# Performance work log

Measured on AMD Instinct MI355X. Metric: run time of the kernel, lower is better.

## Reference

```python
import jax, jax.numpy as jnp
import numpy as np

B, S, D, H = 2, 2048, 1024, 16
DH = D // H  # head_dim = 64


def setup_inputs() -> dict:
    key = jax.random.key(0)
    ks = jax.random.split(key, 12)
    sd = 0.02
    return {
        "query": jax.random.normal(ks[0], (B, S, D), jnp.float32),
        "value": jax.random.normal(ks[1], (B, S, D), jnp.float32),
        "Wq": jax.random.normal(ks[2], (D, D), jnp.float32) * sd,
        "bq": jnp.zeros((D,), jnp.float32),
        "Wk": jax.random.normal(ks[3], (D, DH), jnp.float32) * sd,
        "bk": jnp.zeros((DH,), jnp.float32),
        "Wv": jax.random.normal(ks[4], (D, DH), jnp.float32) * sd,
        "bv": jnp.zeros((DH,), jnp.float32),
        "Wo": jax.random.normal(ks[5], (D, D), jnp.float32) * sd,
        "bo": jnp.zeros((D,), jnp.float32),
    }


def reference(query, value, Wq, bq, Wk, bk, Wv, bv, Wo, bo):
    b, s, d = query.shape
    # per-head queries: (B, H, S, DH)
    Q = (query @ Wq + bq).reshape(b, s, H, DH).transpose(0, 2, 1, 3)
    # single shared K/V head: (B, S, DH)
    K = value @ Wk + bk
    V = value @ Wv + bv
    scale = 1.0 / jnp.sqrt(jnp.asarray(DH, Q.dtype))
    # broadcast shared K over all query heads: (B, H, S, S)
    scores = jnp.einsum("bhsd,btd->bhst", Q, K) * scale
    weights = jax.nn.softmax(scores, axis=-1)
    # (B, H, S, DH)
    attn = jnp.einsum("bhst,btd->bhsd", weights, V)
    concat = attn.transpose(0, 2, 1, 3).reshape(b, s, d)
    return concat @ Wo + bo
```

## Files before the change

### kernel.cpp

```cpp
#include <hip/hip_runtime.h>
#include <hip/hip_bf16.h>
#include <cstdint>

#define S_LEN 2048
#define D_MODEL 1024
#define NHEAD 16
#define DHEAD 64
#define BATCH 2

typedef __attribute__((ext_vector_type(4))) __bf16 bf16x4v;
typedef __attribute__((ext_vector_type(8))) __bf16 bf16x8v;
typedef __attribute__((ext_vector_type(16))) float f32x16;
typedef const __attribute__((address_space(1))) uint32_t gu32;
typedef __attribute__((address_space(3))) uint32_t lu32;

#define QSCALE 0.18033688011112042f

__device__ __forceinline__ int perm4(int gidx) {
    return (gidx & ~3) | ((gidx & 1) << 1) | ((gidx >> 1) & 1);
}
__device__ __forceinline__ int permk(int k) {
    return (k & ~12) | ((k & 4) << 1) | ((k & 8) >> 1);
}

__global__ __launch_bounds__(256) void prep_cvt(
    const float* __restrict__ qin, const float* __restrict__ vin,
    __hip_bfloat16* __restrict__ Qo, __hip_bfloat16* __restrict__ Vo, int n4each)
{
    const int i = blockIdx.x * 256 + threadIdx.x;
    const float* src;
    __hip_bfloat16* dst;
    int idx;
    if (i < n4each) { src = qin; dst = Qo; idx = i; }
    else            { src = vin; dst = Vo; idx = i - n4each; if (idx >= n4each) return; }
    const float4 v = reinterpret_cast<const float4*>(src)[idx];
    bf16x4v o = { (__bf16)v.x, (__bf16)v.y, (__bf16)v.z, (__bf16)v.w };
    *reinterpret_cast<bf16x4v*>(dst + (size_t)perm4(idx) * 4) = o;
}

__global__ __launch_bounds__(256) void wtrans_all(
    const float* __restrict__ Wq, const float* __restrict__ Wo,
    const float* __restrict__ Wk, const float* __restrict__ Wv,
    __hip_bfloat16* __restrict__ Wqt, __hip_bfloat16* __restrict__ Wohit,
    __hip_bfloat16* __restrict__ Wkvt)
{
    const int z = blockIdx.z;
    const float* W;
    __hip_bfloat16* T;
    int wcols, trowoff;
    if (z == 0)      { W = Wq; T = Wqt;   wcols = 1024; trowoff = 0; }
    else if (z == 1) { W = Wo; T = Wohit; wcols = 1024; trowoff = 0; }
    else if (z == 2) { W = Wk; T = Wkvt;  wcols = 64;   trowoff = 0; }
    else             { W = Wv; T = Wkvt;  wcols = 64;   trowoff = 64; }
    const int bx = blockIdx.x, by = blockIdx.y;
    if (bx * 32 >= wcols) return;

    __shared__ float ld[32][33];
    const int tid = threadIdx.x;
    const int jj = tid & 31;
#pragma unroll
    for (int ii = 0; ii < 4; ++ii) {
        const int rr = (tid >> 5) * 4 + ii;
        ld[rr][jj] = W[(size_t)(by * 32 + rr) * wcols + bx * 32 + jj];
    }
    __syncthreads();
#pragma unroll
    for (int ii = 0; ii < 4; ++ii) {
        const int rr = (tid >> 5) * 4 + ii;
        T[(size_t)(trowoff + bx * 32 + rr) * 1024 + by * 32 + permk(jj)] =
            __float2bfloat16(ld[jj][rr]);
    }
}

template<bool FUSED, bool PERMC, typename OutT>
__global__ __launch_bounds__(512, 1) void gemm_mfma(
    const __hip_bfloat16* __restrict__ Ahi, const __hip_bfloat16* __restrict__ Alo,
    const __hip_bfloat16* __restrict__ Bhi,
    const float* __restrict__ bias, OutT* __restrict__ C, float oscale)
{
    constexpr int NT = 16;
    constexpr int NBUF = FUSED ? 3 : 4;
    constexpr int BUFSZ = FUSED ? 49152 : 32768;
    __shared__ __align__(16) char lds[NBUF * BUFSZ];

    const int tid = threadIdx.x;
    const int w = tid >> 6, lane = tid & 63;
    const int g = lane >> 5, r = lane & 31;
    const int wr = w >> 2, wc = w & 3;
    const int lin = blockIdx.y * 8 + blockIdx.x;
    const int swz = (lin & 7) * 32 + (lin >> 3);
    const int rowBase = (swz >> 3) * 128;
    const int colBase = (swz & 7) * 128;

    auto stage = [&](int buf, int t) {
        const int kk = t * 64;
        char* dst = lds + buf * BUFSZ;
#pragma unroll
        for (int j = 0; j < 2; ++j) {
            const int oo  = j * 8192 + tid * 16;
            const int row = oo >> 7;
            const int cb  = (oo & 127) ^ ((row & 7) << 4);
            __builtin_amdgcn_global_load_lds(
                (gu32*)((const char*)Ahi + (size_t)(rowBase + row) * 2048 + kk * 2 + cb),
                (lu32*)(dst + oo), 16, 0, 0);
            if (FUSED)
                __builtin_amdgcn_global_load_lds(
                    (gu32*)((const char*)Alo + (size_t)(rowBase + row) * 2048 + kk * 2 + cb),
                    (lu32*)(dst + 16384 + oo), 16, 0, 0);
            __builtin_amdgcn_global_load_lds(
                (gu32*)((const char*)Bhi + (size_t)(colBase + row) * 2048 + kk * 2 + cb),
                (lu32*)(dst + (FUSED ? 32768 : 16384) + oo), 16, 0, 0);
        }
    };

    f32x16 acc[2];
#pragma unroll
    for (int i = 0; i < 16; ++i) { acc[0][i] = 0.f; acc[1][i] = 0.f; }

    if (FUSED) { stage(0, 0); stage(1, 1); }
    else       { stage(0, 0); stage(1, 1); stage(2, 2); }

    int b_cur = 0, b_nxt = 1, b_stg = 2;

    for (int t = 0; t < NT; ++t) {
        if (FUSED) {
            if (t < 15) { asm volatile("s_waitcnt vmcnt(6)" ::: "memory"); }
            else        { asm volatile("s_waitcnt vmcnt(0)" ::: "memory"); }
        } else {
            if (t <= 13)      { asm volatile("s_waitcnt vmcnt(8)" ::: "memory"); }
            else if (t == 14) { asm volatile("s_waitcnt vmcnt(4)" ::: "memory"); }
            else              { asm volatile("s_waitcnt vmcnt(0)" ::: "memory"); }
        }
        asm volatile("s_barrier" ::: "memory");

        if (FUSED) { if (t + 2 < NT) stage(b_stg, t + 2); }
        else       { if (t + 3 < NT) stage((t + 3) & 3, t + 3); }

        const int cbuf = FUSED ? b_cur : (t & 3);
        const char* ahb = lds + cbuf * BUFSZ;
        const char* alb = ahb + 16384;
        const char* bb  = ahb + (FUSED ? 32768 : 16384);

        __builtin_amdgcn_s_setprio(1);
#pragma unroll
        for (int ks = 0; ks < 4; ++ks) {
            bf16x8v a[2], bfr;
#pragma unroll
            for (int mt = 0; mt < 2; ++mt) {
                const int rowl = wr * 64 + mt * 32 + r;
                const int sz = (rowl & 7) << 4;
                a[mt] = *reinterpret_cast<const bf16x8v*>(
                    ahb + rowl * 128 + ((ks * 32 + g * 16) ^ sz));
            }
            {
                const int rowl = wc * 32 + r;
                const int sz = (rowl & 7) << 4;
                bfr = *reinterpret_cast<const bf16x8v*>(
                    bb + rowl * 128 + ((ks * 32 + g * 16) ^ sz));
            }
#pragma unroll
            for (int mt = 0; mt < 2; ++mt)
                acc[mt] = __builtin_amdgcn_mfma_f32_32x32x16_bf16(a[mt], bfr, acc[mt], 0, 0, 0);
            if (FUSED) {
                bf16x8v a2[2];
#pragma unroll
                for (int mt = 0; mt < 2; ++mt) {
                    const int rowl = wr * 64 + mt * 32 + r;
                    const int sz = (rowl & 7) << 4;
                    a2[mt] = *reinterpret_cast<const bf16x8v*>(
                        alb + rowl * 128 + ((ks * 32 + g * 16) ^ sz));
                }
#pragma unroll
                for (int mt = 0; mt < 2; ++mt)
                    acc[mt] = __builtin_amdgcn_mfma_f32_32x32x16_bf16(a2[mt], bfr, acc[mt], 0, 0, 0);
            }
        }
        __builtin_amdgcn_s_setprio(0);

        if (FUSED) { const int tmp = b_cur; b_cur = b_nxt; b_nxt = b_stg; b_stg = tmp; }
    }

    const int col = colBase + wc * 32 + r;
    const int colp = PERMC ? permk(col) : col;
    const float bv = bias[col];
#pragma unroll
    for (int mt = 0; mt < 2; ++mt)
#pragma unroll
        for (int reg = 0; reg < 16; ++reg) {
            const int row = rowBase + wr * 64 + mt * 32 + (reg & 3) + 8 * (reg >> 2) + 4 * g;
            C[(size_t)row * 1024 + colp] = static_cast<OutT>((acc[mt][reg] + bv) * oscale);
        }
}

__global__ __launch_bounds__(256) void proj_kv_mfma(
    const __hip_bfloat16* __restrict__ Vbf,
    const __hip_bfloat16* __restrict__ Wkvt,
    const float* __restrict__ bk, const float* __restrict__ bv,
    __hip_bfloat16* __restrict__ Kb,
    __hip_bfloat16* __restrict__ Vt)
{
    __shared__ __align__(16) char lds[40960];
    const int tid = threadIdx.x;
    const int w = tid >> 6, lane = tid & 63;
    const int g = lane >> 5, r = lane & 31;
    const int rowBase = blockIdx.x * 32;

    auto stage = [&](int buf, int t) {
        const int kk = t * 64;
        char* dst = lds + buf * 20480;
        {
            const int oo  = tid * 16;
            const int row = oo >> 7;
            const int cb  = (oo & 127) ^ ((row & 7) << 4);
            __builtin_amdgcn_global_load_lds(
                (gu32*)((const char*)Vbf + (size_t)(rowBase + row) * 2048 + kk * 2 + cb),
                (lu32*)(dst + oo), 16, 0, 0);
        }
#pragma unroll
        for (int j = 0; j < 4; ++j) {
            const int oo  = j * 4096 + tid * 16;
            const int row = oo >> 7;
            const int cb  = (oo & 127) ^ ((row & 7) << 4);
            __builtin_amdgcn_global_load_lds(
                (gu32*)((const char*)Wkvt + (size_t)row * 2048 + kk * 2 + cb),
                (lu32*)(dst + 4096 + oo), 16, 0, 0);
        }
    };

    f32x16 acc;
#pragma unroll
    for (int i = 0; i < 16; ++i) acc[i] = 0.f;

    stage(0, 0);

    for (int t = 0; t < 16; ++t) {
        const int cur = t & 1;
        if (t < 15) {
            stage(cur ^ 1, t + 1);
            asm volatile("s_waitcnt vmcnt(5)" ::: "memory");
        } else {
            asm volatile("s_waitcnt vmcnt(0)" ::: "memory");
        }
        asm volatile("s_barrier" ::: "memory");

        const char* ab = lds + cur * 20480;
        const char* bb = ab + 4096;

#pragma unroll
        for (int ks = 0; ks < 4; ++ks) {
            const int sza = (r & 7) << 4;
            bf16x8v af = *reinterpret_cast<const bf16x8v*>(
                ab + r * 128 + ((ks * 32 + g * 16) ^ sza));
            bf16x8v bf = *reinterpret_cast<const bf16x8v*>(
                bb + (w * 32 + r) * 128 + ((ks * 32 + g * 16) ^ sza));
            acc = __builtin_amdgcn_mfma_f32_32x32x16_bf16(af, bf, acc, 0, 0, 0);
        }
        asm volatile("s_barrier" ::: "memory");
    }

    __syncthreads();
    float* ep = reinterpret_cast<float*>(lds);
#pragma unroll
    for (int reg = 0; reg < 16; ++reg) {
        const int m = (reg & 3) + 8 * (reg >> 2) + 4 * g;
        ep[m * 132 + w * 32 + r] = acc[reg];
    }
    __syncthreads();

    {
        const int m  = tid >> 3;
        const int g0 = (tid & 7) * 2;
#pragma unroll
        for (int j = 0; j < 2; ++j) {
            const int gsrc = g0 + j;
            bf16x4v o4;
#pragma unroll
            for (int i2 = 0; i2 < 4; ++i2)
                o4[i2] = (__bf16)(ep[m * 132 + gsrc * 4 + i2] + bk[gsrc * 4 + i2]);
            *reinterpret_cast<bf16x4v*>(
                Kb + (size_t)(rowBase + m) * 64 + perm4(gsrc) * 4) = o4;
        }
    }
    {
        const int vc = tid >> 2;
        const int g0 = (tid & 3) * 2;
        const int batch = rowBase >> 11;
        const float bvv = bv[vc];
#pragma unroll
        for (int j = 0; j < 2; ++j) {
            const int gsrc = g0 + j;
            bf16x4v o4;
#pragma unroll
            for (int i2 = 0; i2 < 4; ++i2)
                o4[i2] = (__bf16)(ep[(gsrc * 4 + i2) * 132 + 64 + vc] + bvv);
            *reinterpret_cast<bf16x4v*>(
                Vt + ((size_t)(batch * 64 + vc)) * 2048 + (rowBase & 2047) + perm4(gsrc) * 4) = o4;
        }
    }
}

__global__ __launch_bounds__(256, 2) void mqa_attn_mfma(
    const __hip_bfloat16* __restrict__ Qbf,
    const __hip_bfloat16* __restrict__ Kbf,
    const __hip_bfloat16* __restrict__ Vt,
    __hip_bfloat16* __restrict__ Ahi,
    __hip_bfloat16* __restrict__ Alo)
{
    __shared__ __align__(16) char lds[65536];

    const int bh = blockIdx.y, b = bh >> 4, h = bh & 15;
    const int qt = blockIdx.x;
    const int tid = threadIdx.x;
    const int w = tid >> 6, lane = tid & 63;
    const int g = lane >> 5, q = lane & 31;

    bf16x8v qf[4];
    {
        const __hip_bfloat16* qp =
            Qbf + ((size_t)(b * S_LEN + qt * 128 + w * 32 + q)) * D_MODEL + h * DHEAD;
#pragma unroll
        for (int ks = 0; ks < 4; ++ks)
            qf[ks] = *reinterpret_cast<const bf16x8v*>(qp + ks * 16 + g * 8);
    }

    const bf16x8v onesf = {(__bf16)1.f, (__bf16)1.f, (__bf16)1.f, (__bf16)1.f,
                           (__bf16)1.f, (__bf16)1.f, (__bf16)1.f, (__bf16)1.f};
    f32x16 fzero;
#pragma unroll
    for (int i = 0; i < 16; ++i) fzero[i] = 0.f;

    const char* kbase = (const char*)Kbf + (size_t)b * S_LEN * DHEAD * 2;
    const char* vbase = (const char*)Vt + (size_t)b * DHEAD * S_LEN * 2;

    auto stage = [&](int buf, int t0) {
        char* dst = lds + buf * 16384;
#pragma unroll
        for (int j = 0; j < 2; ++j) {
            const int oo = j * 4096 + tid * 16;
            const int rr = oo >> 7;
            const int cc = (oo & 127) ^ ((rr & 7) << 4);
            __builtin_amdgcn_global_load_lds(
                (gu32*)(kbase + (size_t)(t0 + rr) * 128 + cc),
                (lu32*)(dst + oo), 16, 0, 0);
            __builtin_amdgcn_global_load_lds(
                (gu32*)(vbase + (size_t)rr * (S_LEN * 2) + t0 * 2 + cc),
                (lu32*)(dst + 8192 + oo), 16, 0, 0);
        }
    };

    f32x16 oacc[2], oacc_l;
#pragma unroll
    for (int i = 0; i < 16; ++i) { oacc[0][i] = 0.f; oacc[1][i] = 0.f; oacc_l[i] = 0.f; }

    auto qkt = [&](f32x16 (&SD)[2], int buf) {
        const char* kb_ = lds + buf * 16384;
#pragma unroll
        for (int mt = 0; mt < 2; ++mt) {
            const int key = mt * 32 + q;
            const char* krow = kb_ + key * 128;
            const int swz = (key & 7) << 4;
            bf16x8v af0 = *reinterpret_cast<const bf16x8v*>(krow + ((g * 16) ^ swz));
            SD[mt] = __builtin_amdgcn_mfma_f32_32x32x16_bf16(af0, qf[0], fzero, 0, 0, 0);
#pragma unroll
            for (int ks = 1; ks < 4; ++ks) {
                bf16x8v af = *reinterpret_cast<const bf16x8v*>(
                    krow + ((ks * 32 + g * 16) ^ swz));
                SD[mt] = __builtin_amdgcn_mfma_f32_32x32x16_bf16(af, qf[ks], SD[mt], 0, 0, 0);
            }
        }
    };

    auto smpv = [&](f32x16 (&SD)[2], int buf) {
#pragma unroll
        for (int mt = 0; mt < 2; ++mt)
#pragma unroll
            for (int r2 = 0; r2 < 16; ++r2)
                SD[mt][r2] = exp2f(SD[mt][r2]);

        bf16x8v pf[4];
#pragma unroll
        for (int ks = 0; ks < 4; ++ks)
#pragma unroll
            for (int e2 = 0; e2 < 8; ++e2)
                pf[ks][e2] = (__bf16)SD[ks >> 1][(ks & 1) * 8 + e2];

        const char* vb_ = lds + buf * 16384 + 8192;
#pragma unroll
        for (int mt = 0; mt < 2; ++mt) {
            const int drow = mt * 32 + q;
            const char* vrow = vb_ + drow * 128;
            const int swz = (drow & 7) << 4;
#pragma unroll
            for (int ks = 0; ks < 4; ++ks) {
                bf16x8v af = *reinterpret_cast<const bf16x8v*>(
                    vrow + ((ks * 32 + g * 16) ^ swz));
                oacc[mt] = __builtin_amdgcn_mfma_f32_32x32x16_bf16(af, pf[ks], oacc[mt], 0, 0, 0);
            }
        }
#pragma unroll
        for (int ks = 0; ks < 4; ++ks)
            oacc_l = __builtin_amdgcn_mfma_f32_32x32x16_bf16(onesf, pf[ks], oacc_l, 0, 0, 0);
    };

    f32x16 sA[2], sB[2];

    stage(0, 0); stage(1, 64); stage(2, 128);
    asm volatile("s_waitcnt vmcnt(8)" ::: "memory");
    asm volatile("s_barrier" ::: "memory");
    qkt(sA, 0);

#define BODY(SB_, TILE_, BQ_, BP_, CUR, NXT, VMCSTR, DOSTAGE)               \
    {                                                                        \
        asm volatile("s_waitcnt vmcnt(" VMCSTR ")" ::: "memory");            \
        asm volatile("s_barrier" ::: "memory");                              \
        if (DOSTAGE) stage(SB_, TILE_);                                      \
        qkt(NXT, BQ_);                                                       \
        smpv(CUR, BP_);                                                      \
    }

    for (int ib = 0; ib < 7; ++ib) {
        const int t4 = ib * 4;
        BODY(3, (t4 + 3) * 64, 1, 0, sA, sB, "4", true);
        BODY(0, (t4 + 4) * 64, 2, 1, sB, sA, "4", true);
        BODY(1, (t4 + 5) * 64, 3, 2, sA, sB, "4", true);
        BODY(2, (t4 + 6) * 64, 0, 3, sB, sA, "4", true);
    }
    BODY(3, 31 * 64, 1, 0, sA, sB, "4", true);
    BODY(0, 0,       2, 1, sB, sA, "4", false);
    BODY(0, 0,       3, 2, sA, sB, "0", false);
#undef BODY
    smpv(sB, 3);

    const float inv = 1.f / oacc_l[0];
    __syncthreads();
    {
        float* ep = reinterpret_cast<float*>(lds) + w * 2080;
#pragma unroll
        for (int mt = 0; mt < 2; ++mt)
#pragma unroll
            for (int r = 0; r < 16; ++r) {
                const int d = mt * 32 + (r & 3) + ((r >> 2) * 8) + g * 4;
                ep[q * 65 + d] = oacc[mt][r] * inv;
            }
    }
    __syncthreads();

    const size_t obase = (size_t)(b * S_LEN + qt * 128) * D_MODEL + h * DHEAD;
    for (int i = tid; i < 128 * 16; i += 256) {
        const int rloc = i >> 4, G = i & 15;
        const float* src = reinterpret_cast<float*>(lds) + (rloc >> 5) * 2080 + (rloc & 31) * 65 + G * 4;
        const size_t o = obase + (size_t)rloc * D_MODEL + perm4(G) * 4;
        bf16x4v hv, lv;
#pragma unroll
        for (int j = 0; j < 4; ++j) {
            const float v = src[j];
            const float h2 = __bfloat162float(__float2bfloat16(v));
            hv[j] = (__bf16)h2;
            lv[j] = (__bf16)(v - h2);
        }
        *reinterpret_cast<bf16x4v*>(Ahi + o) = hv;
        *reinterpret_cast<bf16x4v*>(Alo + o) = lv;
    }
}

extern "C" void kernel_launch(void* const* d_in, const int* in_sizes, int n_in,
                              void* d_out, int out_size, void* d_ws, size_t ws_size,
                              hipStream_t stream)
{
    const float* query = (const float*)d_in[0];
    const float* value = (const float*)d_in[1];
    const float* Wq    = (const float*)d_in[2];
    const float* bq    = (const float*)d_in[3];
    const float* Wk    = (const float*)d_in[4];
    const float* bk    = (const float*)d_in[5];
    const float* Wv    = (const float*)d_in[6];
    const float* bv    = (const float*)d_in[7];
    const float* Wo    = (const float*)d_in[8];
    const float* bo    = (const float*)d_in[9];
    float* out = (float*)d_out;

    const int BS = BATCH * S_LEN;
    char* ws = (char*)d_ws;
    const size_t MB = 1024 * 1024;
    __hip_bfloat16* Qin   = (__hip_bfloat16*)(ws);
    __hip_bfloat16* AhiB  = (__hip_bfloat16*)(ws);
    __hip_bfloat16* Wqt   = (__hip_bfloat16*)(ws + 8 * MB);
    __hip_bfloat16* Vbf   = (__hip_bfloat16*)(ws + 10 * MB);
    __hip_bfloat16* Qbf   = (__hip_bfloat16*)(ws + 10 * MB);
    __hip_bfloat16* AloB  = (__hip_bfloat16*)(ws + 10 * MB);
    __hip_bfloat16* Kbf   = (__hip_bfloat16*)(ws + 18 * MB);
    __hip_bfloat16* Vt    = (__hip_bfloat16*)(ws + 18 * MB + 524288);
    __hip_bfloat16* Wohit = (__hip_bfloat16*)(ws + 19 * MB);
    __hip_bfloat16* Wkvt  = (__hip_bfloat16*)(ws + 21 * MB);

    const int n4each = BS * D_MODEL / 4;
    prep_cvt<<<dim3(2 * n4each / 256), dim3(256), 0, stream>>>(
        query, value, Qin, Vbf, n4each);
    wtrans_all<<<dim3(32, 32, 4), dim3(256), 0, stream>>>(
        Wq, Wo, Wk, Wv, Wqt, Wohit, Wkvt);

    proj_kv_mfma<<<dim3(BS / 32), dim3(256), 0, stream>>>(Vbf, Wkvt, bk, bv, Kbf, Vt);

    gemm_mfma<false, true, __hip_bfloat16><<<dim3(8, 32), dim3(512), 0, stream>>>(
        Qin, Qin, Wqt, bq, Qbf, QSCALE);

    mqa_attn_mfma<<<dim3(S_LEN / 128, BATCH * NHEAD), dim3(256), 0, stream>>>(
        Qbf, Kbf, Vt, AhiB, AloB);

    gemm_mfma<true, false, float><<<dim3(8, 32), dim3(512), 0, stream>>>(
        AhiB, AloB, Wohit, bo, out, 1.0f);
}
```

Measured before the change: 114.5 us.

## Fuse prep kernels and run KV projection alongside Q projection in one launch

Merges the query conversion and weight transposes into a single launch, and drops the separate bf16 conversion of the value input: the KV projection now reads fp32 value directly and converts to bf16 in registers. The KV projection blocks are packed into the same grid as the Q projection GEMM, so both run concurrently in one launch instead of two serial ones. The attention kernel also precomputes its swizzled K/V LDS offsets. This removes two launches and a full fp32-to-bf16 pass over value, at the cost of heterogeneous blocks sharing one large LDS allocation and extra fp32 traffic in the KV blocks.

```diff
diff --git a/kernel.cpp b/kernel.cpp
--- a/kernel.cpp
+++ b/kernel.cpp
@@ -23,28 +23,25 @@
     return (k & ~12) | ((k & 4) << 1) | ((k & 8) >> 1);
 }
 
-__global__ __launch_bounds__(256) void prep_cvt(
-    const float* __restrict__ qin, const float* __restrict__ vin,
-    __hip_bfloat16* __restrict__ Qo, __hip_bfloat16* __restrict__ Vo, int n4each)
-{
-    const int i = blockIdx.x * 256 + threadIdx.x;
-    const float* src;
-    __hip_bfloat16* dst;
-    int idx;
-    if (i < n4each) { src = qin; dst = Qo; idx = i; }
-    else            { src = vin; dst = Vo; idx = i - n4each; if (idx >= n4each) return; }
-    const float4 v = reinterpret_cast<const float4*>(src)[idx];
-    bf16x4v o = { (__bf16)v.x, (__bf16)v.y, (__bf16)v.z, (__bf16)v.w };
-    *reinterpret_cast<bf16x4v*>(dst + (size_t)perm4(idx) * 4) = o;
-}
-
-__global__ __launch_bounds__(256) void wtrans_all(
+__global__ __launch_bounds__(256) void prep_all(
+    const float* __restrict__ query,
     const float* __restrict__ Wq, const float* __restrict__ Wo,
     const float* __restrict__ Wk, const float* __restrict__ Wv,
+    __hip_bfloat16* __restrict__ Qin,
     __hip_bfloat16* __restrict__ Wqt, __hip_bfloat16* __restrict__ Wohit,
     __hip_bfloat16* __restrict__ Wkvt)
 {
-    const int z = blockIdx.z;
+    const int bid = blockIdx.x;
+    const int tid = threadIdx.x;
+    if (bid < 4096) {
+        const int idx = bid * 256 + tid;
+        const float4 v = reinterpret_cast<const float4*>(query)[idx];
+        bf16x4v o = { (__bf16)v.x, (__bf16)v.y, (__bf16)v.z, (__bf16)v.w };
+        *reinterpret_cast<bf16x4v*>(Qin + (size_t)perm4(idx) * 4) = o;
+        return;
+    }
+    const int b2 = bid - 4096;
+    const int bx = b2 & 31, by = (b2 >> 5) & 31, z = b2 >> 10;
     const float* W;
     __hip_bfloat16* T;
     int wcols, trowoff;
@@ -52,11 +49,9 @@
     else if (z == 1) { W = Wo; T = Wohit; wcols = 1024; trowoff = 0; }
     else if (z == 2) { W = Wk; T = Wkvt;  wcols = 64;   trowoff = 0; }
     else             { W = Wv; T = Wkvt;  wcols = 64;   trowoff = 64; }
-    const int bx = blockIdx.x, by = blockIdx.y;
     if (bx * 32 >= wcols) return;
 
     __shared__ float ld[32][33];
-    const int tid = threadIdx.x;
     const int jj = tid & 31;
 #pragma unroll
     for (int ii = 0; ii < 4; ++ii) {
@@ -72,16 +67,216 @@
     }
 }
 
-template<bool FUSED, bool PERMC, typename OutT>
-__global__ __launch_bounds__(512, 1) void gemm_mfma(
+__global__ __launch_bounds__(512, 1) void qproj_projkv(
+    const __hip_bfloat16* __restrict__ Qin,
+    const __hip_bfloat16* __restrict__ Wqt,
+    const float* __restrict__ bq,
+    __hip_bfloat16* __restrict__ Qbf,
+    const float* __restrict__ value,
+    const __hip_bfloat16* __restrict__ Wkvt,
+    const float* __restrict__ bk, const float* __restrict__ bv,
+    __hip_bfloat16* __restrict__ Kb,
+    __hip_bfloat16* __restrict__ Vt)
+{
+    __shared__ __align__(16) char lds[131072];
+    const int bid = blockIdx.x;
+    const int tid = threadIdx.x;
+
+    if (bid < 64) {
+        const int unit = tid >> 8;
+        const int ltid = tid & 255;
+        const int w = ltid >> 6, lane = ltid & 63;
+        const int g = lane >> 5, r = lane & 31;
+        const int rowBase = bid * 64 + unit * 32;
+        char* ub = lds + unit * 65536;
+
+        auto stage = [&](int buf, int t) {
+            const int kk = t * 64;
+            char* dst = ub + buf * 24576;
+#pragma unroll
+            for (int j = 0; j < 2; ++j) {
+                const int oo  = j * 4096 + ltid * 16;
+                const int row = oo >> 8;
+                const int cb  = (oo & 255) ^ ((row & 7) << 4);
+                __builtin_amdgcn_global_load_lds(
+                    (gu32*)((const char*)value + (size_t)(rowBase + row) * 4096 + kk * 4 + cb),
+                    (lu32*)(dst + oo), 16, 0, 0);
+            }
+#pragma unroll
+            for (int j = 0; j < 4; ++j) {
+                const int oo  = j * 4096 + ltid * 16;
+                const int row = oo >> 7;
+                const int cb  = (oo & 127) ^ ((row & 7) << 4);
+                __builtin_amdgcn_global_load_lds(
+                    (gu32*)((const char*)Wkvt + (size_t)row * 2048 + kk * 2 + cb),
+                    (lu32*)(dst + 8192 + oo), 16, 0, 0);
+            }
+        };
+
+        f32x16 acc;
+#pragma unroll
+        for (int i = 0; i < 16; ++i) acc[i] = 0.f;
+
+        stage(0, 0);
+
+        for (int t = 0; t < 16; ++t) {
+            const int cur = t & 1;
+            if (t < 15) {
+                stage(cur ^ 1, t + 1);
+                asm volatile("s_waitcnt vmcnt(6)" ::: "memory");
+            } else {
+                asm volatile("s_waitcnt vmcnt(0)" ::: "memory");
+            }
+            asm volatile("s_barrier" ::: "memory");
+
+            const char* ab = ub + cur * 24576;
+            const char* bb = ab + 8192;
+
+#pragma unroll
+            for (int ks = 0; ks < 4; ++ks) {
+                const int sza = (r & 7) << 4;
+                const char* pa = ab + r * 256;
+                const float4 x0 = *reinterpret_cast<const float4*>(
+                    pa + ((ks * 64 + g * 16) ^ sza));
+                const float4 x1 = *reinterpret_cast<const float4*>(
+                    pa + ((ks * 64 + 32 + g * 16) ^ sza));
+                bf16x8v af = {(__bf16)x0.x, (__bf16)x0.y, (__bf16)x0.z, (__bf16)x0.w,
+                              (__bf16)x1.x, (__bf16)x1.y, (__bf16)x1.z, (__bf16)x1.w};
+                bf16x8v bf = *reinterpret_cast<const bf16x8v*>(
+                    bb + (w * 32 + r) * 128 + ((ks * 32 + g * 16) ^ sza));
+                acc = __builtin_amdgcn_mfma_f32_32x32x16_bf16(af, bf, acc, 0, 0, 0);
+            }
+            asm volatile("s_barrier" ::: "memory");
+        }
+
+        __syncthreads();
+        float* ep = reinterpret_cast<float*>(ub);
+#pragma unroll
+        for (int reg = 0; reg < 16; ++reg) {
+            const int m = (reg & 3) + 8 * (reg >> 2) + 4 * g;
+            ep[m * 132 + w * 32 + r] = acc[reg];
+        }
+        __syncthreads();
+
+        {
+            const int m  = ltid >> 3;
+            const int g0 = (ltid & 7) * 2;
+#pragma unroll
+            for (int j = 0; j < 2; ++j) {
+                const int gsrc = g0 + j;
+                bf16x4v o4;
+#pragma unroll
+                for (int i2 = 0; i2 < 4; ++i2)
+                    o4[i2] = (__bf16)(ep[m * 132 + gsrc * 4 + i2] + bk[gsrc * 4 + i2]);
+                *reinterpret_cast<bf16x4v*>(
+                    Kb + (size_t)(rowBase + m) * 64 + perm4(gsrc) * 4) = o4;
+            }
+        }
+        {
+            const int vc = ltid >> 2;
+            const int g0 = (ltid & 3) * 2;
+            const int batch = rowBase >> 11;
+            const float bvv = bv[vc];
+#pragma unroll
+            for (int j = 0; j < 2; ++j) {
+                const int gsrc = g0 + j;
+                bf16x4v o4;
+#pragma unroll
+                for (int i2 = 0; i2 < 4; ++i2)
+                    o4[i2] = (__bf16)(ep[(gsrc * 4 + i2) * 132 + 64 + vc] + bvv);
+                *reinterpret_cast<bf16x4v*>(
+                    Vt + ((size_t)(batch * 64 + vc)) * 2048 + (rowBase & 2047) + perm4(gsrc) * 4) = o4;
+            }
+        }
+        return;
+    }
+
+    const int lin = bid - 64;
+    const int w = tid >> 6, lane = tid & 63;
+    const int g = lane >> 5, r = lane & 31;
+    const int wr = w >> 2, wc = w & 3;
+    const int swz = (lin & 7) * 32 + (lin >> 3);
+    const int rowBase = (swz >> 3) * 128;
+    const int colBase = (swz & 7) * 128;
+
+    auto stage = [&](int buf, int t) {
+        const int kk = t * 64;
+        char* dst = lds + buf * 32768;
+#pragma unroll
+        for (int j = 0; j < 2; ++j) {
+            const int oo  = j * 8192 + tid * 16;
+            const int row = oo >> 7;
+            const int cb  = (oo & 127) ^ ((row & 7) << 4);
+            __builtin_amdgcn_global_load_lds(
+                (gu32*)((const char*)Qin + (size_t)(rowBase + row) * 2048 + kk * 2 + cb),
+                (lu32*)(dst + oo), 16, 0, 0);
+            __builtin_amdgcn_global_load_lds(
+                (gu32*)((const char*)Wqt + (size_t)(colBase + row) * 2048 + kk * 2 + cb),
+                (lu32*)(dst + 16384 + oo), 16, 0, 0);
+        }
+    };
+
+    f32x16 acc[2];
+#pragma unroll
+    for (int i = 0; i < 16; ++i) { acc[0][i] = 0.f; acc[1][i] = 0.f; }
+
+    stage(0, 0); stage(1, 1); stage(2, 2);
+
+    for (int t = 0; t < 16; ++t) {
+        if (t <= 13)      { asm volatile("s_waitcnt vmcnt(8)" ::: "memory"); }
+        else if (t == 14) { asm volatile("s_waitcnt vmcnt(4)" ::: "memory"); }
+        else              { asm volatile("s_waitcnt vmcnt(0)" ::: "memory"); }
+        asm volatile("s_barrier" ::: "memory");
+
+        if (t + 3 < 16) stage((t + 3) & 3, t + 3);
+
+        const char* ahb = lds + (t & 3) * 32768;
+        const char* bb  = ahb + 16384;
+
+        __builtin_amdgcn_s_setprio(1);
+#pragma unroll
+        for (int ks = 0; ks < 4; ++ks) {
+            bf16x8v a[2], bfr;
+#pragma unroll
+            for (int mt = 0; mt < 2; ++mt) {
+                const int rowl = wr * 64 + mt * 32 + r;
+                const int sz = (rowl & 7) << 4;
+                a[mt] = *reinterpret_cast<const bf16x8v*>(
+                    ahb + rowl * 128 + ((ks * 32 + g * 16) ^ sz));
+            }
+            {
+                const int rowl = wc * 32 + r;
+                const int sz = (rowl & 7) << 4;
+                bfr = *reinterpret_cast<const bf16x8v*>(
+                    bb + rowl * 128 + ((ks * 32 + g * 16) ^ sz));
+            }
+#pragma unroll
+            for (int mt = 0; mt < 2; ++mt)
+                acc[mt] = __builtin_amdgcn_mfma_f32_32x32x16_bf16(a[mt], bfr, acc[mt], 0, 0, 0);
+        }
+        __builtin_amdgcn_s_setprio(0);
+    }
+
+    const int col = colBase + wc * 32 + r;
+    const int colp = permk(col);
+    const float bvv = bq[col];
+#pragma unroll
+    for (int mt = 0; mt < 2; ++mt)
+#pragma unroll
+        for (int reg = 0; reg < 16; ++reg) {
+            const int row = rowBase + wr * 64 + mt * 32 + (reg & 3) + 8 * (reg >> 2) + 4 * g;
+            Qbf[(size_t)row * 1024 + colp] =
+                (__hip_bfloat16)((acc[mt][reg] + bvv) * QSCALE);
+        }
+}
+
+__global__ __launch_bounds__(512, 1) void gemm_oproj(
     const __hip_bfloat16* __restrict__ Ahi, const __hip_bfloat16* __restrict__ Alo,
     const __hip_bfloat16* __restrict__ Bhi,
-    const float* __restrict__ bias, OutT* __restrict__ C, float oscale)
+    const float* __restrict__ bias, float* __restrict__ C)
 {
-    constexpr int NT = 16;
-    constexpr int NBUF = FUSED ? 3 : 4;
-    constexpr int BUFSZ = FUSED ? 49152 : 32768;
-    __shared__ __align__(16) char lds[NBUF * BUFSZ];
+    constexpr int BUFSZ = 49152;
+    __shared__ __align__(16) char lds[147456];
 
     const int tid = threadIdx.x;
     const int w = tid >> 6, lane = tid & 63;
@@ -103,13 +298,12 @@
             __builtin_amdgcn_global_load_lds(
                 (gu32*)((const char*)Ahi + (size_t)(rowBase + row) * 2048 + kk * 2 + cb),
                 (lu32*)(dst + oo), 16, 0, 0);
-            if (FUSED)
-                __builtin_amdgcn_global_load_lds(
-                    (gu32*)((const char*)Alo + (size_t)(rowBase + row) * 2048 + kk * 2 + cb),
-                    (lu32*)(dst + 16384 + oo), 16, 0, 0);
+            __builtin_amdgcn_global_load_lds(
+                (gu32*)((const char*)Alo + (size_t)(rowBase + row) * 2048 + kk * 2 + cb),
+                (lu32*)(dst + 16384 + oo), 16, 0, 0);
             __builtin_amdgcn_global_load_lds(
                 (gu32*)((const char*)Bhi + (size_t)(colBase + row) * 2048 + kk * 2 + cb),
-                (lu32*)(dst + (FUSED ? 32768 : 16384) + oo), 16, 0, 0);
+                (lu32*)(dst + 32768 + oo), 16, 0, 0);
         }
     };
 
@@ -117,40 +311,32 @@
 #pragma unroll
     for (int i = 0; i < 16; ++i) { acc[0][i] = 0.f; acc[1][i] = 0.f; }
 
-    if (FUSED) { stage(0, 0); stage(1, 1); }
-    else       { stage(0, 0); stage(1, 1); stage(2, 2); }
-
+    stage(0, 0); stage(1, 1);
     int b_cur = 0, b_nxt = 1, b_stg = 2;
 
-    for (int t = 0; t < NT; ++t) {
-        if (FUSED) {
-            if (t < 15) { asm volatile("s_waitcnt vmcnt(6)" ::: "memory"); }
-            else        { asm volatile("s_waitcnt vmcnt(0)" ::: "memory"); }
-        } else {
-            if (t <= 13)      { asm volatile("s_waitcnt vmcnt(8)" ::: "memory"); }
-            else if (t == 14) { asm volatile("s_waitcnt vmcnt(4)" ::: "memory"); }
-            else              { asm volatile("s_waitcnt vmcnt(0)" ::: "memory"); }
-        }
+    for (int t = 0; t < 16; ++t) {
+        if (t < 15) { asm volatile("s_waitcnt vmcnt(6)" ::: "memory"); }
+        else        { asm volatile("s_waitcnt vmcnt(0)" ::: "memory"); }
         asm volatile("s_barrier" ::: "memory");
 
-        if (FUSED) { if (t + 2 < NT) stage(b_stg, t + 2); }
-        else       { if (t + 3 < NT) stage((t + 3) & 3, t + 3); }
-
-        const int cbuf = FUSED ? b_cur : (t & 3);
-        const char* ahb = lds + cbuf * BUFSZ;
+        if (t + 2 < 16) stage(b_stg, t + 2);
+
+        const char* ahb = lds + b_cur * BUFSZ;
         const char* alb = ahb + 16384;
-        const char* bb  = ahb + (FUSED ? 32768 : 16384);
+        const char* bb  = ahb + 32768;
 
         __builtin_amdgcn_s_setprio(1);
 #pragma unroll
         for (int ks = 0; ks < 4; ++ks) {
-            bf16x8v a[2], bfr;
+            bf16x8v a[2], a2[2], bfr;
 #pragma unroll
             for (int mt = 0; mt < 2; ++mt) {
                 const int rowl = wr * 64 + mt * 32 + r;
                 const int sz = (rowl & 7) << 4;
-                a[mt] = *reinterpret_cast<const bf16x8v*>(
+                a[mt]  = *reinterpret_cast<const bf16x8v*>(
                     ahb + rowl * 128 + ((ks * 32 + g * 16) ^ sz));
+                a2[mt] = *reinterpret_cast<const bf16x8v*>(
+                    alb + rowl * 128 + ((ks * 32 + g * 16) ^ sz));
             }
             {
                 const int rowl = wc * 32 + r;
@@ -159,144 +345,25 @@
                     bb + rowl * 128 + ((ks * 32 + g * 16) ^ sz));
             }
 #pragma unroll
-            for (int mt = 0; mt < 2; ++mt)
-                acc[mt] = __builtin_amdgcn_mfma_f32_32x32x16_bf16(a[mt], bfr, acc[mt], 0, 0, 0);
-            if (FUSED) {
-                bf16x8v a2[2];
-#pragma unroll
-                for (int mt = 0; mt < 2; ++mt) {
-                    const int rowl = wr * 64 + mt * 32 + r;
-                    const int sz = (rowl & 7) << 4;
-                    a2[mt] = *reinterpret_cast<const bf16x8v*>(
-                        alb + rowl * 128 + ((ks * 32 + g * 16) ^ sz));
-                }
-#pragma unroll
-                for (int mt = 0; mt < 2; ++mt)
-                    acc[mt] = __builtin_amdgcn_mfma_f32_32x32x16_bf16(a2[mt], bfr, acc[mt], 0, 0, 0);
+            for (int mt = 0; mt < 2; ++mt) {
+                acc[mt] = __builtin_amdgcn_mfma_f32_32x32x16_bf16(a[mt],  bfr, acc[mt], 0, 0, 0);
+                acc[mt] = __builtin_amdgcn_mfma_f32_32x32x16_bf16(a2[mt], bfr, acc[mt], 0, 0, 0);
             }
         }
         __builtin_amdgcn_s_setprio(0);
 
-        if (FUSED) { const int tmp = b_cur; b_cur = b_nxt; b_nxt = b_stg; b_stg = tmp; }
+        const int tmp = b_cur; b_cur = b_nxt; b_nxt = b_stg; b_stg = tmp;
     }
 
     const int col = colBase + wc * 32 + r;
-    const int colp = PERMC ? permk(col) : col;
-    const float bv = bias[col];
+    const float bvv = bias[col];
 #pragma unroll
     for (int mt = 0; mt < 2; ++mt)
 #pragma unroll
         for (int reg = 0; reg < 16; ++reg) {
             const int row = rowBase + wr * 64 + mt * 32 + (reg & 3) + 8 * (reg >> 2) + 4 * g;
-            C[(size_t)row * 1024 + colp] = static_cast<OutT>((acc[mt][reg] + bv) * oscale);
-        }
-}
-
-__global__ __launch_bounds__(256) void proj_kv_mfma(
-    const __hip_bfloat16* __restrict__ Vbf,
-    const __hip_bfloat16* __restrict__ Wkvt,
-    const float* __restrict__ bk, const float* __restrict__ bv,
-    __hip_bfloat16* __restrict__ Kb,
-    __hip_bfloat16* __restrict__ Vt)
-{
-    __shared__ __align__(16) char lds[40960];
-    const int tid = threadIdx.x;
-    const int w = tid >> 6, lane = tid & 63;
-    const int g = lane >> 5, r = lane & 31;
-    const int rowBase = blockIdx.x * 32;
-
-    auto stage = [&](int buf, int t) {
-        const int kk = t * 64;
-        char* dst = lds + buf * 20480;
-        {
-            const int oo  = tid * 16;
-            const int row = oo >> 7;
-            const int cb  = (oo & 127) ^ ((row & 7) << 4);
-            __builtin_amdgcn_global_load_lds(
-                (gu32*)((const char*)Vbf + (size_t)(rowBase + row) * 2048 + kk * 2 + cb),
-                (lu32*)(dst + oo), 16, 0, 0);
-        }
-#pragma unroll
-        for (int j = 0; j < 4; ++j) {
-            const int oo  = j * 4096 + tid * 16;
-            const int row = oo >> 7;
-            const int cb  = (oo & 127) ^ ((row & 7) << 4);
-            __builtin_amdgcn_global_load_lds(
-                (gu32*)((const char*)Wkvt + (size_t)row * 2048 + kk * 2 + cb),
-                (lu32*)(dst + 4096 + oo), 16, 0, 0);
-        }
-    };
-
-    f32x16 acc;
-#pragma unroll
-    for (int i = 0; i < 16; ++i) acc[i] = 0.f;
-
-    stage(0, 0);
-
-    for (int t = 0; t < 16; ++t) {
-        const int cur = t & 1;
-        if (t < 15) {
-            stage(cur ^ 1, t + 1);
-            asm volatile("s_waitcnt vmcnt(5)" ::: "memory");
-        } else {
-            asm volatile("s_waitcnt vmcnt(0)" ::: "memory");
-        }
-        asm volatile("s_barrier" ::: "memory");
-
-        const char* ab = lds + cur * 20480;
-        const char* bb = ab + 4096;
-
-#pragma unroll
-        for (int ks = 0; ks < 4; ++ks) {
-            const int sza = (r & 7) << 4;
-            bf16x8v af = *reinterpret_cast<const bf16x8v*>(
-                ab + r * 128 + ((ks * 32 + g * 16) ^ sza));
-            bf16x8v bf = *reinterpret_cast<const bf16x8v*>(
-                bb + (w * 32 + r) * 128 + ((ks * 32 + g * 16) ^ sza));
-            acc = __builtin_amdgcn_mfma_f32_32x32x16_bf16(af, bf, acc, 0, 0, 0);
-        }
-        asm volatile("s_barrier" ::: "memory");
-    }
-
-    __syncthreads();
-    float* ep = reinterpret_cast<float*>(lds);
-#pragma unroll
-    for (int reg = 0; reg < 16; ++reg) {
-        const int m = (reg & 3) + 8 * (reg >> 2) + 4 * g;
-        ep[m * 132 + w * 32 + r] = acc[reg];
-    }
-    __syncthreads();
-
-    {
-        const int m  = tid >> 3;
-        const int g0 = (tid & 7) * 2;
-#pragma unroll
-        for (int j = 0; j < 2; ++j) {
-            const int gsrc = g0 + j;
-            bf16x4v o4;
-#pragma unroll
-            for (int i2 = 0; i2 < 4; ++i2)
-                o4[i2] = (__bf16)(ep[m * 132 + gsrc * 4 + i2] + bk[gsrc * 4 + i2]);
-            *reinterpret_cast<bf16x4v*>(
-                Kb + (size_t)(rowBase + m) * 64 + perm4(gsrc) * 4) = o4;
-        }
-    }
-    {
-        const int vc = tid >> 2;
-        const int g0 = (tid & 3) * 2;
-        const int batch = rowBase >> 11;
-        const float bvv = bv[vc];
-#pragma unroll
-        for (int j = 0; j < 2; ++j) {
-            const int gsrc = g0 + j;
-            bf16x4v o4;
-#pragma unroll
-            for (int i2 = 0; i2 < 4; ++i2)
-                o4[i2] = (__bf16)(ep[(gsrc * 4 + i2) * 132 + 64 + vc] + bvv);
-            *reinterpret_cast<bf16x4v*>(
-                Vt + ((size_t)(batch * 64 + vc)) * 2048 + (rowBase & 2047) + perm4(gsrc) * 4) = o4;
-        }
-    }
+            C[(size_t)row * 1024 + col] = acc[mt][reg] + bvv;
+        }
 }
 
 __global__ __launch_bounds__(256, 2) void mqa_attn_mfma(
@@ -329,6 +396,18 @@
 #pragma unroll
     for (int i = 0; i < 16; ++i) fzero[i] = 0.f;
 
+    int koff[2][4], voff[2][4];
+#pragma unroll
+    for (int mt = 0; mt < 2; ++mt) {
+        const int key = mt * 32 + q;
+        const int swzk = (key & 7) << 4;
+#pragma unroll
+        for (int ks = 0; ks < 4; ++ks) {
+            koff[mt][ks] = key * 128 + ((ks * 32 + g * 16) ^ swzk);
+            voff[mt][ks] = 8192 + key * 128 + ((ks * 32 + g * 16) ^ swzk);
+        }
+    }
+
     const char* kbase = (const char*)Kbf + (size_t)b * S_LEN * DHEAD * 2;
     const char* vbase = (const char*)Vt + (size_t)b * DHEAD * S_LEN * 2;
 
@@ -356,15 +435,11 @@
         const char* kb_ = lds + buf * 16384;
 #pragma unroll
         for (int mt = 0; mt < 2; ++mt) {
-            const int key = mt * 32 + q;
-            const char* krow = kb_ + key * 128;
-            const int swz = (key & 7) << 4;
-            bf16x8v af0 = *reinterpret_cast<const bf16x8v*>(krow + ((g * 16) ^ swz));
+            bf16x8v af0 = *reinterpret_cast<const bf16x8v*>(kb_ + koff[mt][0]);
             SD[mt] = __builtin_amdgcn_mfma_f32_32x32x16_bf16(af0, qf[0], fzero, 0, 0, 0);
 #pragma unroll
             for (int ks = 1; ks < 4; ++ks) {
-                bf16x8v af = *reinterpret_cast<const bf16x8v*>(
-                    krow + ((ks * 32 + g * 16) ^ swz));
+                bf16x8v af = *reinterpret_cast<const bf16x8v*>(kb_ + koff[mt][ks]);
                 SD[mt] = __builtin_amdgcn_mfma_f32_32x32x16_bf16(af, qf[ks], SD[mt], 0, 0, 0);
             }
         }
@@ -384,16 +459,12 @@
             for (int e2 = 0; e2 < 8; ++e2)
                 pf[ks][e2] = (__bf16)SD[ks >> 1][(ks & 1) * 8 + e2];
 
-        const char* vb_ = lds + buf * 16384 + 8192;
+        const char* kb_ = lds + buf * 16384;
 #pragma unroll
         for (int mt = 0; mt < 2; ++mt) {
-            const int drow = mt * 32 + q;
-            const char* vrow = vb_ + drow * 128;
-            const int swz = (drow & 7) << 4;
 #pragma unroll
             for (int ks = 0; ks < 4; ++ks) {
-                bf16x8v af = *reinterpret_cast<const bf16x8v*>(
-                    vrow + ((ks * 32 + g * 16) ^ swz));
+                bf16x8v af = *reinterpret_cast<const bf16x8v*>(kb_ + voff[mt][ks]);
                 oacc[mt] = __builtin_amdgcn_mfma_f32_32x32x16_bf16(af, pf[ks], oacc[mt], 0, 0, 0);
             }
         }
@@ -479,13 +550,11 @@
     const float* bo    = (const float*)d_in[9];
     float* out = (float*)d_out;
 
-    const int BS = BATCH * S_LEN;
     char* ws = (char*)d_ws;
     const size_t MB = 1024 * 1024;
     __hip_bfloat16* Qin   = (__hip_bfloat16*)(ws);
     __hip_bfloat16* AhiB  = (__hip_bfloat16*)(ws);
     __hip_bfloat16* Wqt   = (__hip_bfloat16*)(ws + 8 * MB);
-    __hip_bfloat16* Vbf   = (__hip_bfloat16*)(ws + 10 * MB);
     __hip_bfloat16* Qbf   = (__hip_bfloat16*)(ws + 10 * MB);
     __hip_bfloat16* AloB  = (__hip_bfloat16*)(ws + 10 * MB);
     __hip_bfloat16* Kbf   = (__hip_bfloat16*)(ws + 18 * MB);
@@ -493,20 +562,15 @@
     __hip_bfloat16* Wohit = (__hip_bfloat16*)(ws + 19 * MB);
     __hip_bfloat16* Wkvt  = (__hip_bfloat16*)(ws + 21 * MB);
 
-    const int n4each = BS * D_MODEL / 4;
-    prep_cvt<<<dim3(2 * n4each / 256), dim3(256), 0, stream>>>(
-        query, value, Qin, Vbf, n4each);
-    wtrans_all<<<dim3(32, 32, 4), dim3(256), 0, stream>>>(
-        Wq, Wo, Wk, Wv, Wqt, Wohit, Wkvt);
-
-    proj_kv_mfma<<<dim3(BS / 32), dim3(256), 0, stream>>>(Vbf, Wkvt, bk, bv, Kbf, Vt);
-
-    gemm_mfma<false, true, __hip_bfloat16><<<dim3(8, 32), dim3(512), 0, stream>>>(
-        Qin, Qin, Wqt, bq, Qbf, QSCALE);
+    prep_all<<<dim3(8192), dim3(256), 0, stream>>>(
+        query, Wq, Wo, Wk, Wv, Qin, Wqt, Wohit, Wkvt);
+
+    qproj_projkv<<<dim3(320), dim3(512), 0, stream>>>(
+        Qin, Wqt, bq, Qbf, value, Wkvt, bk, bv, Kbf, Vt);
 
     mqa_attn_mfma<<<dim3(S_LEN / 128, BATCH * NHEAD), dim3(256), 0, stream>>>(
         Qbf, Kbf, Vt, AhiB, AloB);
 
-    gemm_mfma<true, false, float><<<dim3(8, 32), dim3(512), 0, stream>>>(
-        AhiB, AloB, Wohit, bo, out, 1.0f);
-}
+    gemm_oproj<<<dim3(8, 32), dim3(512), 0, stream>>>(
+        AhiB, AloB, Wohit, bo, out);
+}
```

Measured after the change: 109.3 us. 1.05x faster.
